# Kernel optimization log

Hardware: AMD Instinct MI355X
Metric: run time of the kernel (lower is better)

The kernel has to match this reference:

```python
import jax, jax.numpy as jnp
import numpy as np

DIM = 768
HEADS = 12
K_PARTS = 64
MLP_HIDDEN = 4 * DIM
EPS = 1e-5


def layer_norm(x, g, b):
    mu = jnp.mean(x, axis=-1, keepdims=True)
    var = jnp.mean(jnp.square(x - mu), axis=-1, keepdims=True)
    return (x - mu) * jax.lax.rsqrt(var + EPS) * g + b


def attention(x, qkv_w, qkv_b, proj_w, proj_b, num_heads):
    B, N, C = x.shape
    hd = C // num_heads
    scale = hd ** -0.5
    qkv = x @ qkv_w.T + qkv_b                      # (B,N,3C)
    qkv = qkv.reshape(B, N, 3, num_heads, hd).transpose(2, 0, 3, 1, 4)  # (3,B,H,N,hd)
    q, k, v = qkv[0], qkv[1], qkv[2]
    attn = jax.nn.softmax(jnp.einsum('bhqd,bhkd->bhqk', q, k) * scale, axis=-1)
    out = jnp.einsum('bhqk,bhkd->bhqd', attn, v)   # (B,H,N,hd)
    out = out.transpose(0, 2, 1, 3).reshape(B, N, C)
    return out @ proj_w.T + proj_b, attn


def mlp(x, fc1_w, fc1_b, fc2_w, fc2_b):
    h = jax.nn.gelu(x @ fc1_w.T + fc1_b, approximate=False)
    return h @ fc2_w.T + fc2_b


def setup_inputs() -> dict:
    key = jax.random.key(0)
    ks = jax.random.split(key, 16)
    s = lambda fan_in: 1.0 / np.sqrt(fan_in)
    inp = {
        'x': jax.random.normal(ks[0], (8, 1024, DIM), dtype=jnp.float32),
        'ln1_g': jnp.ones((DIM,), jnp.float32),
        'ln1_b': jnp.zeros((DIM,), jnp.float32),
        'qkv_w': jax.random.normal(ks[1], (3 * DIM, DIM), jnp.float32) * s(DIM),
        'qkv_b': jnp.zeros((3 * DIM,), jnp.float32),
        'proj_w': jax.random.normal(ks[2], (DIM, DIM), jnp.float32) * s(DIM),
        'proj_b': jnp.zeros((DIM,), jnp.float32),
        'c_qkv_w': jax.random.normal(ks[3], (3 * DIM, DIM), jnp.float32) * s(DIM),
        'c_qkv_b': jnp.zeros((3 * DIM,), jnp.float32),
        'c_proj_w': jax.random.normal(ks[4], (DIM, DIM), jnp.float32) * s(DIM),
        'c_proj_b': jnp.zeros((DIM,), jnp.float32),
        'cp_fc1_w': jax.random.normal(ks[5], (K_PARTS, K_PARTS), jnp.float32) * s(K_PARTS),
        'cp_fc1_b': jnp.zeros((K_PARTS,), jnp.float32),
        'cp_fc2_w': jax.random.normal(ks[6], (DIM, K_PARTS), jnp.float32) * s(K_PARTS),
        'cp_fc2_b': jnp.zeros((DIM,), jnp.float32),
        'P': jax.random.normal(ks[7], (K_PARTS, DIM), jnp.float32),
        'ln2_g': jnp.ones((DIM,), jnp.float32),
        'ln2_b': jnp.zeros((DIM,), jnp.float32),
        'fc1_w': jax.random.normal(ks[8], (MLP_HIDDEN, DIM), jnp.float32) * s(DIM),
        'fc1_b': jnp.zeros((MLP_HIDDEN,), jnp.float32),
        'fc2_w': jax.random.normal(ks[9], (DIM, MLP_HIDDEN), jnp.float32) * s(MLP_HIDDEN),
        'fc2_b': jnp.zeros((DIM,), jnp.float32),
    }
    # normalize P rows like the module init (F.normalize(orthogonal, dim=-1))
    inp['P'] = inp['P'] / jnp.linalg.norm(inp['P'], axis=-1, keepdims=True)
    return inp


def reference(x, ln1_g, ln1_b, qkv_w, qkv_b, proj_w, proj_b,
              c_qkv_w, c_qkv_b, c_proj_w, c_proj_b,
              cp_fc1_w, cp_fc1_b, cp_fc2_w, cp_fc2_b, P,
              ln2_g, ln2_b, fc1_w, fc1_b, fc2_w, fc2_b):
    n1 = layer_norm(x, ln1_g, ln1_b)
    y, _ = attention(n1, qkv_w, qkv_b, proj_w, proj_b, HEADS)
    # SimilarityMaps: L2-normalize tokens and parts, cosine similarity map (B,N,K)
    Un = n1 / jnp.linalg.norm(n1, axis=-1, keepdims=True)
    Pn = P / jnp.linalg.norm(P, axis=-1, keepdims=True)
    dmap = jnp.einsum('bnd,kd->bnk', Un, Pn)
    # c_project: Mlp K -> K -> dim, then parts attention
    zin = mlp(dmap, cp_fc1_w, cp_fc1_b, cp_fc2_w, cp_fc2_b)
    z, _ = attention(zin, c_qkv_w, c_qkv_b, c_proj_w, c_proj_b, HEADS)
    x = x + y + z                                  # gamma_1 is None, drop_path=0
    x = x + mlp(layer_norm(x, ln2_g, ln2_b), fc1_w, fc1_b, fc2_w, fc2_b)
    return x, dmap
```

## Files before the change

kernel.cpp:

```cpp
#include <hip/hip_runtime.h>


typedef unsigned short u16;
typedef unsigned int   u32;
typedef __attribute__((ext_vector_type(8))) short short8;
typedef __attribute__((ext_vector_type(8))) unsigned short ushort8v;
typedef __attribute__((ext_vector_type(4))) float f32x4;

#define F_GELU     1
#define F_ROWSCALE 2
#define F_RES1     4
#define F_RESF     8
#define F_OUTB     16
#define F_OUTF     32
#define F_BIAS     64

__device__ __forceinline__ float bf2f(u32 b) { return __uint_as_float(b << 16); }
__device__ __forceinline__ u16 f2bf(float f) {
    u32 u = __float_as_uint(f);
    u32 r = u + 0x7fffu + ((u >> 16) & 1u);
    return (u16)(r >> 16);
}
__device__ __forceinline__ u16 f2bf_fast(float f) {
    return (u16)((__float_as_uint(f) + 0x8000u) >> 16);
}
__device__ __forceinline__ float gelu_exact(float v) {
    return 0.5f * v * (1.0f + erff(v * 0.70710678118654752440f));
}
__device__ __forceinline__ float gelu_fast(float x) {
    float u = 0.79788456080286535588f * (x + 0.044715f * x * x * x);
    float e = __builtin_amdgcn_exp2f(u * 2.88539008177792681472f);
    float t = 1.0f - 2.0f / (e + 1.0f);
    return 0.5f * x * (1.0f + t);
}

__device__ __forceinline__ void gload16(const u16* g, u16* l) {
    __builtin_amdgcn_global_load_lds(
        (const __attribute__((address_space(1))) u32*)g,
        (__attribute__((address_space(3))) u32*)l, 16, 0, 0);
}

struct ConvArgs {
    const float* src[8];
    u16*         dst[8];
    int          nblk[9];
    int          n[8];
};

__global__ __launch_bounds__(256)
void conv_all_k(ConvArgs a)
{
    const int b = blockIdx.x;
    int i = 0;
    #pragma unroll
    for (int j = 0; j < 7; j++) if (b >= a.nblk[j + 1]) i = j + 1;
    const int base = (b - a.nblk[i]) * 1024 + threadIdx.x * 4;
    if (base >= a.n[i]) return;
    float4 v = *(const float4*)(a.src[i] + base);
    ushort4 o;
    o.x = f2bf(v.x); o.y = f2bf(v.y); o.z = f2bf(v.z); o.w = f2bf(v.w);
    *(ushort4*)(a.dst[i] + base) = o;
}

__device__ __forceinline__ float block_sum(float v, float* red) {
    #pragma unroll
    for (int off = 32; off > 0; off >>= 1) v += __shfl_down(v, off);
    __syncthreads();
    if ((threadIdx.x & 63) == 0) red[threadIdx.x >> 6] = v;
    __syncthreads();
    return red[0] + red[1] + red[2] + red[3];
}

template<bool NORM>
__global__ __launch_bounds__(256)
void ln_k(const float* __restrict__ xin, const float* __restrict__ g,
          const float* __restrict__ bta, u16* __restrict__ out,
          float* __restrict__ invnorm)
{
    __shared__ float red[4];
    const int row = blockIdx.x, t = threadIdx.x;
    float v[3];
    #pragma unroll
    for (int i = 0; i < 3; i++)
        v[i] = xin[(size_t)row * 768 + t + i * 256];
    float tot = block_sum(v[0] + v[1] + v[2], red);
    float mu  = tot * (1.0f / 768.0f);
    float d0 = v[0] - mu, d1 = v[1] - mu, d2 = v[2] - mu;
    float tot2 = block_sum(d0 * d0 + d1 * d1 + d2 * d2, red);
    float rstd = rsqrtf(tot2 * (1.0f / 768.0f) + 1e-5f);
    float ss = 0.0f;
    #pragma unroll
    for (int i = 0; i < 3; i++) {
        int c = t + i * 256;
        float yy = (v[i] - mu) * rstd * g[c] + bta[c];
        out[(size_t)row * 768 + c] = f2bf(yy);
        ss += yy * yy;
    }
    if constexpr (NORM) {
        float tot3 = block_sum(ss, red);
        if (t == 0) invnorm[row] = rsqrtf(tot3);
    }
}

__global__ __launch_bounds__(256)
void pn_k(const float* __restrict__ P, u16* __restrict__ Pn)
{
    __shared__ float red[4];
    const int row = blockIdx.x, t = threadIdx.x;
    float v[3];
    #pragma unroll
    for (int i = 0; i < 3; i++)
        v[i] = P[(size_t)row * 768 + t + i * 256];
    float tot = block_sum(v[0]*v[0] + v[1]*v[1] + v[2]*v[2], red);
    float inv = rsqrtf(tot);
    #pragma unroll
    for (int i = 0; i < 3; i++)
        Pn[(size_t)row * 768 + t + i * 256] = f2bf(v[i] * inv);
}

template<int FLAGS>
__global__ __launch_bounds__(256)
void gemm_mfma(const u16* __restrict__ A, const u16* __restrict__ W,
               const float* __restrict__ bias,
               const u16* __restrict__ res1, const float* __restrict__ resf,
               u16* __restrict__ out, float* __restrict__ outf,
               int M, int N, int K)
{
    __shared__ u16 smem[3][8192];
    const int t = threadIdx.x;
    const int wave = t >> 6, lane = t & 63;
    const int nbx  = gridDim.x;
    const int orig = blockIdx.x + blockIdx.y * nbx;
    const int cpx  = (nbx * gridDim.y) >> 3;
    const int xcd  = orig & 7, loc = orig >> 3;
    const int Rc   = cpx / nbx;
    const int gsz  = 6 * Rc;
    const int grp  = loc / gsz;
    const int rem  = loc - grp * gsz;
    const int ccol = grp * 6 + rem % 6;
    const int crow = xcd * Rc + rem / 6;
    const int m0 = crow * 128, n0 = ccol * 128;
    const int Wm = (wave >> 1) * 64, Wn = (wave & 1) * 64;
    const int rr = lane >> 2, cc = (lane & 3) * 8;
    const int quad = lane >> 4, r16 = lane & 15;
    const int NK = K >> 5;

    f32x4 acc[4][4];
    #pragma unroll
    for (int i = 0; i < 4; i++)
        #pragma unroll
        for (int j = 0; j < 4; j++)
            acc[i][j] = (f32x4){0.f, 0.f, 0.f, 0.f};

    #pragma unroll
    for (int c = 0; c < 2; c++) {
        const int chunk = wave * 2 + c;
        const int row = chunk * 16 + rr;
        gload16(A + (size_t)(m0 + row) * K + cc, &smem[0][chunk * 512]);
        gload16(W + (size_t)(n0 + row) * K + cc, &smem[0][4096 + chunk * 512]);
    }
    if (NK > 1) {
        #pragma unroll
        for (int c = 0; c < 2; c++) {
            const int chunk = wave * 2 + c;
            const int row = chunk * 16 + rr;
            gload16(A + (size_t)(m0 + row) * K + 32 + cc, &smem[1][chunk * 512]);
            gload16(W + (size_t)(n0 + row) * K + 32 + cc, &smem[1][4096 + chunk * 512]);
        }
    }

    for (int kt = 0; kt < NK; kt++) {
        const int cur = kt % 3;
        if (kt + 1 < NK)
            asm volatile("s_waitcnt vmcnt(4)\n\ts_barrier" ::: "memory");
        else
            asm volatile("s_waitcnt vmcnt(0)\n\ts_barrier" ::: "memory");
        if (kt + 2 < NK) {
            const int k0 = (kt + 2) * 32;
            const int nb = (kt + 2) % 3;
            #pragma unroll
            for (int c = 0; c < 2; c++) {
                const int chunk = wave * 2 + c;
                const int row = chunk * 16 + rr;
                gload16(A + (size_t)(m0 + row) * K + k0 + cc,
                        &smem[nb][chunk * 512]);
                gload16(W + (size_t)(n0 + row) * K + k0 + cc,
                        &smem[nb][4096 + chunk * 512]);
            }
        }
        short8 af[4], bfr[4];
        #pragma unroll
        for (int i = 0; i < 4; i++) {
            af[i]  = *(const short8*)&smem[cur][(Wm + i * 16 + r16) * 32 + quad * 8];
            bfr[i] = *(const short8*)&smem[cur][4096 + (Wn + i * 16 + r16) * 32 + quad * 8];
        }
        #pragma unroll
        for (int i = 0; i < 4; i++)
            #pragma unroll
            for (int j = 0; j < 4; j++)
                acc[i][j] = __builtin_amdgcn_mfma_f32_16x16x32_bf16(
                    af[i], bfr[j], acc[i][j], 0, 0, 0);
    }
    __syncthreads();

    float* myl = (float*)&smem[0][0] + wave * 1088;
    float bj[4];
    #pragma unroll
    for (int j = 0; j < 4; j++) {
        if constexpr (FLAGS & F_BIAS) bj[j] = bias[n0 + Wn + j * 16 + r16];
        else bj[j] = 0.0f;
    }
    const int row = lane >> 2, seg = (lane & 3) * 16;

    #pragma unroll
    for (int i = 0; i < 4; i++) {
        #pragma unroll
        for (int j = 0; j < 4; j++)
            #pragma unroll
            for (int r = 0; r < 4; r++) {
                float v = acc[i][j][r] + bj[j];
                if constexpr (FLAGS & F_GELU) v = gelu_fast(v);
                myl[(quad * 4 + r) * 68 + j * 16 + r16] = v;
            }
        float v[16];
        #pragma unroll
        for (int k4 = 0; k4 < 4; k4++) {
            float4 f = *(const float4*)&myl[row * 68 + seg + k4 * 4];
            v[k4 * 4 + 0] = f.x; v[k4 * 4 + 1] = f.y;
            v[k4 * 4 + 2] = f.z; v[k4 * 4 + 3] = f.w;
        }
        const int m = m0 + Wm + i * 16 + row;
        const size_t idx = (size_t)m * N + n0 + Wn + seg;
        if constexpr (FLAGS & F_RES1) {
            ushort8v r0 = *(const ushort8v*)(res1 + idx);
            ushort8v r1 = *(const ushort8v*)(res1 + idx + 8);
            #pragma unroll
            for (int k = 0; k < 8; k++) { v[k] += bf2f(r0[k]); v[k + 8] += bf2f(r1[k]); }
        }
        if constexpr (FLAGS & F_RESF) {
            #pragma unroll
            for (int k4 = 0; k4 < 4; k4++) {
                float4 f = *(const float4*)(resf + idx + k4 * 4);
                v[k4 * 4 + 0] += f.x; v[k4 * 4 + 1] += f.y;
                v[k4 * 4 + 2] += f.z; v[k4 * 4 + 3] += f.w;
            }
        }
        if constexpr (FLAGS & F_OUTB) {
            ushort8v o0, o1;
            #pragma unroll
            for (int k = 0; k < 8; k++) { o0[k] = f2bf(v[k]); o1[k] = f2bf(v[k + 8]); }
            *(ushort8v*)(out + idx) = o0;
            *(ushort8v*)(out + idx + 8) = o1;
        }
        if constexpr (FLAGS & F_OUTF) {
            #pragma unroll
            for (int k4 = 0; k4 < 4; k4++) {
                float4 f = {v[k4 * 4 + 0], v[k4 * 4 + 1], v[k4 * 4 + 2], v[k4 * 4 + 3]};
                *(float4*)(outf + idx + k4 * 4) = f;
            }
        }
    }
}

template<int BM, int BN, int FLAGS>
__global__ __launch_bounds__(256)
void gemm_k(const u16* __restrict__ A, const u16* __restrict__ W,
            const float* __restrict__ bias, const float* __restrict__ rowscale,
            const u16* __restrict__ res1, const float* __restrict__ resf,
            u16* __restrict__ out, float* __restrict__ outf,
            int M, int N, int K)
{
    constexpr int RM = BM / 16, RN = BN / 16;
    __shared__ float Asm[16][BM + 4];
    __shared__ float Wsm[16][BN + 4];
    const int t  = threadIdx.x;
    const int tx = t & 15, ty = t >> 4;
    const int m0 = blockIdx.y * BM, n0 = blockIdx.x * BN;

    float acc[RM][RN];
    #pragma unroll
    for (int i = 0; i < RM; i++)
        #pragma unroll
        for (int j = 0; j < RN; j++) acc[i][j] = 0.0f;

    for (int k0 = 0; k0 < K; k0 += 16) {
        #pragma unroll
        for (int i = 0; i < BM / 64; i++) {
            int f = t + i * 256, r = f >> 2, c4 = (f & 3) << 2;
            uint2 u = *(const uint2*)(A + (size_t)(m0 + r) * K + k0 + c4);
            Asm[c4 + 0][r] = bf2f(u.x & 0xffffu);
            Asm[c4 + 1][r] = bf2f(u.x >> 16);
            Asm[c4 + 2][r] = bf2f(u.y & 0xffffu);
            Asm[c4 + 3][r] = bf2f(u.y >> 16);
        }
        #pragma unroll
        for (int i = 0; i < BN / 64; i++) {
            int f = t + i * 256, r = f >> 2, c4 = (f & 3) << 2;
            uint2 u = *(const uint2*)(W + (size_t)(n0 + r) * K + k0 + c4);
            Wsm[c4 + 0][r] = bf2f(u.x & 0xffffu);
            Wsm[c4 + 1][r] = bf2f(u.x >> 16);
            Wsm[c4 + 2][r] = bf2f(u.y & 0xffffu);
            Wsm[c4 + 3][r] = bf2f(u.y >> 16);
        }
        __syncthreads();
        #pragma unroll
        for (int k = 0; k < 16; k++) {
            float a[RM], w[RN];
            #pragma unroll
            for (int ii = 0; ii < RM; ii += 4) {
                float4 v = *(const float4*)&Asm[k][ty * RM + ii];
                a[ii] = v.x; a[ii + 1] = v.y; a[ii + 2] = v.z; a[ii + 3] = v.w;
            }
            #pragma unroll
            for (int jj = 0; jj < RN; jj += 4) {
                float4 v = *(const float4*)&Wsm[k][tx * RN + jj];
                w[jj] = v.x; w[jj + 1] = v.y; w[jj + 2] = v.z; w[jj + 3] = v.w;
            }
            #pragma unroll
            for (int i = 0; i < RM; i++)
                #pragma unroll
                for (int j = 0; j < RN; j++)
                    acc[i][j] = fmaf(a[i], w[j], acc[i][j]);
        }
        __syncthreads();
    }

    #pragma unroll
    for (int i = 0; i < RM; i++) {
        const int m = m0 + ty * RM + i;
        float rs = 1.0f;
        if constexpr (FLAGS & F_ROWSCALE) rs = rowscale[m];
        #pragma unroll
        for (int jj = 0; jj < RN; jj += 4) {
            const int n = n0 + tx * RN + jj;
            const size_t idx = (size_t)m * N + n;
            float b4[4] = {0.f, 0.f, 0.f, 0.f};
            if constexpr (FLAGS & F_BIAS) {
                float4 bvv = *(const float4*)(bias + n);
                b4[0] = bvv.x; b4[1] = bvv.y; b4[2] = bvv.z; b4[3] = bvv.w;
            }
            float e[4];
            #pragma unroll
            for (int j = 0; j < 4; j++) {
                float v = acc[i][jj + j];
                if constexpr (FLAGS & F_BIAS) v += b4[j];
                if constexpr (FLAGS & F_GELU) v = gelu_exact(v);
                if constexpr (FLAGS & F_ROWSCALE) v *= rs;
                e[j] = v;
            }
            if constexpr (FLAGS & F_OUTB) {
                ushort4 o4;
                o4.x = f2bf(e[0]); o4.y = f2bf(e[1]);
                o4.z = f2bf(e[2]); o4.w = f2bf(e[3]);
                *(ushort4*)(out + idx) = o4;
            }
            if constexpr (FLAGS & F_OUTF) {
                float4 o4 = {e[0], e[1], e[2], e[3]};
                *(float4*)(outf + idx) = o4;
            }
        }
    }
}

__global__ __launch_bounds__(256)
void attn_mfma(const u16* __restrict__ qkv, u16* __restrict__ out)
{
    const int orig = blockIdx.x + blockIdx.y * 8;
    const int wg   = (orig & 7) * 96 + (orig >> 3);
    const int qt = wg & 7;
    const int bh = wg >> 3;
    const int b = bh / 12, h = bh % 12;
    __shared__ u16 Qs[2 * 128 * 32];
    __shared__ u16 Ks[2 * 64 * 32];
    __shared__ u16 Vt[2 * 64 * 32];
    __shared__ u16 Ps[2 * 128 * 32];
    const int t = threadIdx.x;
    const int wave = t >> 6, lane = t & 63;
    const int quad = lane >> 4, r16 = lane & 15;
    const size_t RS = 2304;
    const int tok0 = b * 1024 + qt * 128;
    const u16* qbase = qkv + (size_t)tok0 * RS + h * 64;
    const float SC = 0.125f * 1.44269504088896340736f;

    #pragma unroll
    for (int c = 0; c < 4; c++) {
        int idx = wave * 4 + c;
        int kc = idx >> 3, rg = idx & 7;
        int row = rg * 16 + (lane >> 2);
        gload16(qbase + (size_t)row * RS + kc * 32 + (lane & 3) * 8,
                &Qs[kc * 4096 + rg * 512]);
    }

    f32x4 O[2][4];
    float lpart[2][4];
    #pragma unroll
    for (int i = 0; i < 2; i++)
        #pragma unroll
        for (int j = 0; j < 4; j++) {
            O[i][j] = (f32x4){0.f, 0.f, 0.f, 0.f};
            lpart[i][j & 3] = 0.0f;
        }

    const int kp = t & 63, dg = t >> 6;
    const int vb = (kp >> 5) * 2048 + (kp & 31);
    uint2 vr[4];

    {
        const u16* kbase = qkv + (size_t)(b * 1024) * RS + 768 + h * 64;
        #pragma unroll
        for (int c = 0; c < 2; c++) {
            int idx = wave * 2 + c;
            int kc = idx >> 2, rg = idx & 3;
            int row = rg * 16 + (lane >> 2);
            gload16(kbase + (size_t)row * RS + kc * 32 + (lane & 3) * 8,
                    &Ks[kc * 2048 + rg * 512]);
        }
        const u16* vbase = qkv + (size_t)(b * 1024) * RS + 1536 + h * 64;
        #pragma unroll
        for (int it = 0; it < 4; it++) {
            int d0 = dg * 16 + it * 4;
            vr[it] = *(const uint2*)(vbase + (size_t)kp * RS + d0);
        }
    }

    for (int kt = 0; kt < 16; kt++) {
        __syncthreads();
        #pragma unroll
        for (int it = 0; it < 4; it++) {
            int d0 = dg * 16 + it * 4;
            uint2 u = vr[it];
            Vt[vb + (d0 + 0) * 32] = (u16)(u.x & 0xffffu);
            Vt[vb + (d0 + 1) * 32] = (u16)(u.x >> 16);
            Vt[vb + (d0 + 2) * 32] = (u16)(u.y & 0xffffu);
            Vt[vb + (d0 + 3) * 32] = (u16)(u.y >> 16);
        }

        f32x4 S[2][4];
        #pragma unroll
        for (int i = 0; i < 2; i++)
            #pragma unroll
            for (int j = 0; j < 4; j++)
                S[i][j] = (f32x4){0.f, 0.f, 0.f, 0.f};
        __builtin_amdgcn_s_setprio(1);
        #pragma unroll
        for (int kc = 0; kc < 2; kc++) {
            short8 aq[2], bk[4];
            #pragma unroll
            for (int i = 0; i < 2; i++)
                aq[i] = *(const short8*)&Qs[kc * 4096 + (wave * 32 + i * 16 + r16) * 32 + quad * 8];
            #pragma unroll
            for (int j = 0; j < 4; j++)
                bk[j] = *(const short8*)&Ks[kc * 2048 + (j * 16 + r16) * 32 + quad * 8];
            #pragma unroll
            for (int i = 0; i < 2; i++)
                #pragma unroll
                for (int j = 0; j < 4; j++)
                    S[i][j] = __builtin_amdgcn_mfma_f32_16x16x32_bf16(
                        aq[i], bk[j], S[i][j], 0, 0, 0);
        }
        __builtin_amdgcn_s_setprio(0);

        #pragma unroll
        for (int i = 0; i < 2; i++) {
            #pragma unroll
            for (int j = 0; j < 4; j++) {
                const int col = j * 16 + r16;
                const int pb = (col >> 5) * 4096 + (col & 31);
                #pragma unroll
                for (int r = 0; r < 4; r++) {
                    float p = __builtin_amdgcn_exp2f(S[i][j][r] * SC);
                    lpart[i][r] += p;
                    const int row = wave * 32 + i * 16 + quad * 4 + r;
                    Ps[pb + row * 32] = f2bf_fast(p);
                }
            }
        }

        __syncthreads();

        if (kt < 15) {
            const u16* kbase = qkv + (size_t)(b * 1024 + (kt + 1) * 64) * RS + 768 + h * 64;
            #pragma unroll
            for (int c = 0; c < 2; c++) {
                int idx = wave * 2 + c;
                int kc = idx >> 2, rg = idx & 3;
                int row = rg * 16 + (lane >> 2);
                gload16(kbase + (size_t)row * RS + kc * 32 + (lane & 3) * 8,
                        &Ks[kc * 2048 + rg * 512]);
            }
            const u16* vbase = qkv + (size_t)(b * 1024 + (kt + 1) * 64) * RS + 1536 + h * 64;
            #pragma unroll
            for (int it = 0; it < 4; it++) {
                int d0 = dg * 16 + it * 4;
                vr[it] = *(const uint2*)(vbase + (size_t)kp * RS + d0);
            }
        }

        __builtin_amdgcn_s_setprio(1);
        #pragma unroll
        for (int kc = 0; kc < 2; kc++) {
            short8 ap[2], bv[4];
            #pragma unroll
            for (int i = 0; i < 2; i++)
                ap[i] = *(const short8*)&Ps[kc * 4096 + (wave * 32 + i * 16 + r16) * 32 + quad * 8];
            #pragma unroll
            for (int j = 0; j < 4; j++)
                bv[j] = *(const short8*)&Vt[kc * 2048 + (j * 16 + r16) * 32 + quad * 8];
            #pragma unroll
            for (int i = 0; i < 2; i++)
                #pragma unroll
                for (int j = 0; j < 4; j++)
                    O[i][j] = __builtin_amdgcn_mfma_f32_16x16x32_bf16(
                        ap[i], bv[j], O[i][j], 0, 0, 0);
        }
        __builtin_amdgcn_s_setprio(0);
    }

    const int row = lane >> 2, seg = (lane & 3) * 16;
    #pragma unroll
    for (int i = 0; i < 2; i++) {
        float linv[4];
        #pragma unroll
        for (int r = 0; r < 4; r++) {
            float l = lpart[i][r];
            l += __shfl_xor(l, 1);
            l += __shfl_xor(l, 2);
            l += __shfl_xor(l, 4);
            l += __shfl_xor(l, 8);
            linv[r] = 1.0f / l;
        }
        u16* myl = &Ps[wave * 2048 + i * 1024];
        #pragma unroll
        for (int j = 0; j < 4; j++)
            #pragma unroll
            for (int r = 0; r < 4; r++)
                myl[(quad * 4 + r) * 64 + j * 16 + r16] = f2bf(O[i][j][r] * linv[r]);
        const int token = tok0 + wave * 32 + i * 16 + row;
        const size_t oidx = (size_t)token * 768 + h * 64 + seg;
        *(ushort8v*)(out + oidx)     = *(const ushort8v*)&myl[row * 64 + seg];
        *(ushort8v*)(out + oidx + 8) = *(const ushort8v*)&myl[row * 64 + seg + 8];
    }
}

extern "C" void kernel_launch(void* const* d_in, const int* in_sizes, int n_in,
                              void* d_out, int out_size, void* d_ws, size_t ws_size,
                              hipStream_t stream)
{
    (void)in_sizes; (void)n_in; (void)out_size; (void)ws_size;
    const float* x        = (const float*)d_in[0];
    const float* ln1_g    = (const float*)d_in[1];
    const float* ln1_b    = (const float*)d_in[2];
    const float* qkv_w    = (const float*)d_in[3];
    const float* qkv_b    = (const float*)d_in[4];
    const float* proj_w   = (const float*)d_in[5];
    const float* proj_b   = (const float*)d_in[6];
    const float* c_qkv_w  = (const float*)d_in[7];
    const float* c_qkv_b  = (const float*)d_in[8];
    const float* c_proj_w = (const float*)d_in[9];
    const float* c_proj_b = (const float*)d_in[10];
    const float* cp_fc1_w = (const float*)d_in[11];
    const float* cp_fc1_b = (const float*)d_in[12];
    const float* cp_fc2_w = (const float*)d_in[13];
    const float* cp_fc2_b = (const float*)d_in[14];
    const float* P        = (const float*)d_in[15];
    const float* ln2_g    = (const float*)d_in[16];
    const float* ln2_b    = (const float*)d_in[17];
    const float* fc1_w    = (const float*)d_in[18];
    const float* fc1_b    = (const float*)d_in[19];
    const float* fc2_w    = (const float*)d_in[20];
    const float* fc2_b    = (const float*)d_in[21];

    float* out_x    = (float*)d_out;
    float* out_dmap = out_x + 6291456;

    u16* us    = (u16*)d_ws;
    u16* n1n2  = us;
    u16* bigA  = us + 6291456;
    u16* ao    = bigA + 18874368;
    u16* y     = us + 31457280;
    float* xs  = (float*)(us + 37748736);
    u16* dmapb = us + 50331648;
    u16* cph   = us + 50855936;
    u16* Pn    = us + 51380224;
    float* invn = (float*)(us + 51429376);
    u16* ci    = us + 51445760;

    u16* w_qkv   = ci;
    u16* w_proj  = ci + 1769472;
    u16* w_cqkv  = ci + 2359296;
    u16* w_cproj = ci + 4128768;
    u16* w_cpf1  = ci + 4718592;
    u16* w_cpf2  = ci + 4722688;
    u16* w_fc1   = ci + 4771840;
    u16* w_fc2   = ci + 7131136;

    {
        ConvArgs a;
        const float* wsrc[8] = { qkv_w, proj_w, c_qkv_w, c_proj_w,
                                 cp_fc1_w, cp_fc2_w, fc1_w, fc2_w };
        u16* wdst[8] = { w_qkv, w_proj, w_cqkv, w_cproj,
                         w_cpf1, w_cpf2, w_fc1, w_fc2 };
        const int wn[8] = { 1769472, 589824, 1769472, 589824,
                            4096, 49152, 2359296, 2359296 };
        int cum = 0;
        for (int i = 0; i < 8; i++) {
            a.src[i] = wsrc[i]; a.dst[i] = wdst[i]; a.n[i] = wn[i];
            a.nblk[i] = cum;
            cum += (wn[i] / 4 + 255) / 256;
        }
        a.nblk[8] = cum;
        conv_all_k<<<cum, 256, 0, stream>>>(a);
    }

    pn_k<<<64, 256, 0, stream>>>(P, Pn);
    ln_k<true><<<8192, 256, 0, stream>>>(x, ln1_g, ln1_b, n1n2, invn);
    gemm_mfma<F_BIAS | F_OUTB>
        <<<dim3(18, 64), 256, 0, stream>>>(n1n2, w_qkv, qkv_b, nullptr, nullptr,
                                           bigA, nullptr, 8192, 2304, 768);
    attn_mfma<<<dim3(8, 96), 256, 0, stream>>>(bigA, ao);
    gemm_mfma<F_BIAS | F_OUTB>
        <<<dim3(6, 64), 256, 0, stream>>>(ao, w_proj, proj_b, nullptr, nullptr,
                                          y, nullptr, 8192, 768, 768);
    gemm_k<64, 64, F_ROWSCALE | F_OUTB | F_OUTF>
        <<<dim3(1, 128), 256, 0, stream>>>(n1n2, Pn, nullptr, invn, nullptr,
                                           nullptr, dmapb, out_dmap, 8192, 64, 768);
    gemm_k<64, 64, F_BIAS | F_GELU | F_OUTB>
        <<<dim3(1, 128), 256, 0, stream>>>(dmapb, w_cpf1, cp_fc1_b, nullptr,
                                           nullptr, nullptr, cph, nullptr, 8192, 64, 64);
    gemm_mfma<F_BIAS | F_OUTB>
        <<<dim3(6, 64), 256, 0, stream>>>(cph, w_cpf2, cp_fc2_b, nullptr, nullptr,
                                          n1n2, nullptr, 8192, 768, 64);
    gemm_mfma<F_BIAS | F_OUTB>
        <<<dim3(18, 64), 256, 0, stream>>>(n1n2, w_cqkv, c_qkv_b, nullptr, nullptr,
                                           bigA, nullptr, 8192, 2304, 768);
    attn_mfma<<<dim3(8, 96), 256, 0, stream>>>(bigA, ao);
    gemm_mfma<F_BIAS | F_RES1 | F_RESF | F_OUTF>
        <<<dim3(6, 64), 256, 0, stream>>>(ao, w_cproj, c_proj_b, y, x,
                                          nullptr, xs, 8192, 768, 768);
    ln_k<false><<<8192, 256, 0, stream>>>(xs, ln2_g, ln2_b, n1n2, nullptr);
    gemm_mfma<F_BIAS | F_GELU | F_OUTB>
        <<<dim3(24, 64), 256, 0, stream>>>(n1n2, w_fc1, fc1_b, nullptr, nullptr,
                                           bigA, nullptr, 8192, 3072, 768);
    gemm_mfma<F_BIAS | F_RESF | F_OUTF>
        <<<dim3(6, 64), 256, 0, stream>>>(bigA, w_fc2, fc2_b, nullptr, xs,
                                          nullptr, out_x, 8192, 768, 3072);
}
```

Before: 545.4 us.

## Add 256x256-tile 512-thread MFMA GEMM for QKV and FC1 projections

Adds a new bf16 MFMA GEMM kernel with 256x256 output tiles, 8 waves, double-buffered swizzled LDS, direct global-to-LDS loads and XCD-aware block mapping. It replaces the smaller-tile GEMM for the two QKV projections and FC1. The aim is more data reuse per tile and fewer global loads per FLOP on these large-N GEMMs. The tradeoff is fewer blocks (288/384), which may underfill the GPU's CUs and cause tail effects, plus heavy register use from 128 accumulators per thread.

New measurement: 588.3 us. 7.9% more time.

```diff
diff --git a/kernel.cpp b/kernel.cpp
--- a/kernel.cpp
+++ b/kernel.cpp
@@ -116,6 +116,140 @@
     #pragma unroll
     for (int i = 0; i < 3; i++)
         Pn[(size_t)row * 768 + t + i * 256] = f2bf(v[i] * inv);
+}
+
+template<int FLAGS>
+__global__ __launch_bounds__(512, 2)
+void gemm256(const u16* __restrict__ A, const u16* __restrict__ W,
+             const float* __restrict__ bias, u16* __restrict__ out,
+             int M, int N, int K)
+{
+    __shared__ u16 As[2][16384];
+    __shared__ u16 Bs[2][16384];
+    const int t = threadIdx.x;
+    const int wave = t >> 6, lane = t & 63;
+    const int quad = lane >> 4, r16 = lane & 15;
+    const int wr = wave >> 2, wc = wave & 3;
+
+    const int nbx = gridDim.x, nby = gridDim.y;
+    const int orig = blockIdx.x + blockIdx.y * nbx;
+    const int Rc   = nby >> 3;
+    const int xcd  = orig & 7, loc = orig >> 3;
+    const int m0 = (xcd * Rc + (loc % Rc)) * 256;
+    const int n0 = (loc / Rc) * 256;
+    const int NT = K >> 6;
+
+    f32x4 acc[8][4];
+    #pragma unroll
+    for (int i = 0; i < 8; i++)
+        #pragma unroll
+        for (int j = 0; j < 4; j++)
+            acc[i][j] = (f32x4){0.f, 0.f, 0.f, 0.f};
+
+    const int srow = wave * 8 + (lane >> 3);
+    const int scol = ((lane & 7) ^ ((lane >> 3) & 7)) * 8;
+
+    const u16* Abase = A + (size_t)m0 * K;
+    const u16* Wbase = W + (size_t)n0 * K;
+
+    #pragma unroll
+    for (int i = 0; i < 4; i++)
+        gload16(Abase + (size_t)(i * 64 + srow) * K + scol,
+                &As[0][i * 4096 + wave * 512]);
+    #pragma unroll
+    for (int i = 0; i < 4; i++)
+        gload16(Wbase + (size_t)(i * 64 + srow) * K + scol,
+                &Bs[0][i * 4096 + wave * 512]);
+    if (NT > 1) {
+        #pragma unroll
+        for (int i = 0; i < 4; i++)
+            gload16(Abase + (size_t)(i * 64 + srow) * K + 64 + scol,
+                    &As[1][i * 4096 + wave * 512]);
+        #pragma unroll
+        for (int i = 0; i < 4; i++)
+            gload16(Wbase + (size_t)(i * 64 + srow) * K + 64 + scol,
+                    &Bs[1][i * 4096 + wave * 512]);
+    }
+
+    for (int kt = 0; kt < NT; kt++) {
+        const int c = kt & 1;
+        if (kt + 1 < NT)
+            asm volatile("s_waitcnt vmcnt(8)\n\ts_barrier" ::: "memory");
+        else
+            asm volatile("s_waitcnt vmcnt(0)\n\ts_barrier" ::: "memory");
+
+        #pragma unroll
+        for (int ks = 0; ks < 2; ks++) {
+            short8 bfr[4], af[8];
+            #pragma unroll
+            for (int j = 0; j < 4; j++) {
+                const int br = wc * 64 + j * 16 + r16;
+                bfr[j] = *(const short8*)
+                    &Bs[c][br * 64 + (((ks * 4 + quad) ^ (br & 7)) * 8)];
+            }
+            #pragma unroll
+            for (int i = 0; i < 8; i++) {
+                const int ar = wr * 128 + i * 16 + r16;
+                af[i] = *(const short8*)
+                    &As[c][ar * 64 + (((ks * 4 + quad) ^ (ar & 7)) * 8)];
+            }
+            __builtin_amdgcn_s_setprio(1);
+            #pragma unroll
+            for (int i = 0; i < 8; i++)
+                #pragma unroll
+                for (int j = 0; j < 4; j++)
+                    acc[i][j] = __builtin_amdgcn_mfma_f32_16x16x32_bf16(
+                        af[i], bfr[j], acc[i][j], 0, 0, 0);
+            __builtin_amdgcn_s_setprio(0);
+        }
+        asm volatile("s_barrier" ::: "memory");
+        if (kt + 2 < NT) {
+            const int k0 = (kt + 2) * 64;
+            #pragma unroll
+            for (int i = 0; i < 4; i++)
+                gload16(Abase + (size_t)(i * 64 + srow) * K + k0 + scol,
+                        &As[c][i * 4096 + wave * 512]);
+            #pragma unroll
+            for (int i = 0; i < 4; i++)
+                gload16(Wbase + (size_t)(i * 64 + srow) * K + k0 + scol,
+                        &Bs[c][i * 4096 + wave * 512]);
+        }
+    }
+
+    float* myl = (float*)&As[0][0] + wave * 1088;
+    float bj[4];
+    #pragma unroll
+    for (int j = 0; j < 4; j++) {
+        if constexpr (FLAGS & F_BIAS) bj[j] = bias[n0 + wc * 64 + j * 16 + r16];
+        else bj[j] = 0.0f;
+    }
+    const int row = lane >> 2, seg = (lane & 3) * 16;
+
+    #pragma unroll
+    for (int i = 0; i < 8; i++) {
+        #pragma unroll
+        for (int j = 0; j < 4; j++)
+            #pragma unroll
+            for (int r = 0; r < 4; r++) {
+                float v = acc[i][j][r] + bj[j];
+                if constexpr (FLAGS & F_GELU) v = gelu_fast(v);
+                myl[(quad * 4 + r) * 68 + j * 16 + r16] = v;
+            }
+        float v[16];
+        #pragma unroll
+        for (int k4 = 0; k4 < 4; k4++) {
+            float4 f = *(const float4*)&myl[row * 68 + seg + k4 * 4];
+            v[k4 * 4 + 0] = f.x; v[k4 * 4 + 1] = f.y;
+            v[k4 * 4 + 2] = f.z; v[k4 * 4 + 3] = f.w;
+        }
+        const int m = m0 + wr * 128 + i * 16 + row;
+        const size_t idx = (size_t)m * N + n0 + wc * 64 + seg;
+        ushort8v o0, o1;
+        #pragma unroll
+        for (int k = 0; k < 8; k++) { o0[k] = f2bf(v[k]); o1[k] = f2bf(v[k + 8]); }
+        *(ushort8v*)(out + idx) = o0;
+        *(ushort8v*)(out + idx + 8) = o1;
+    }
 }
 
 template<int FLAGS>
@@ -614,9 +748,9 @@
 
     pn_k<<<64, 256, 0, stream>>>(P, Pn);
     ln_k<true><<<8192, 256, 0, stream>>>(x, ln1_g, ln1_b, n1n2, invn);
-    gemm_mfma<F_BIAS | F_OUTB>
-        <<<dim3(18, 64), 256, 0, stream>>>(n1n2, w_qkv, qkv_b, nullptr, nullptr,
-                                           bigA, nullptr, 8192, 2304, 768);
+    gemm256<F_BIAS | F_OUTB>
+        <<<dim3(9, 32), 512, 0, stream>>>(n1n2, w_qkv, qkv_b, bigA,
+                                          8192, 2304, 768);
     attn_mfma<<<dim3(8, 96), 256, 0, stream>>>(bigA, ao);
     gemm_mfma<F_BIAS | F_OUTB>
         <<<dim3(6, 64), 256, 0, stream>>>(ao, w_proj, proj_b, nullptr, nullptr,
@@ -630,17 +764,17 @@
     gemm_mfma<F_BIAS | F_OUTB>
         <<<dim3(6, 64), 256, 0, stream>>>(cph, w_cpf2, cp_fc2_b, nullptr, nullptr,
                                           n1n2, nullptr, 8192, 768, 64);
-    gemm_mfma<F_BIAS | F_OUTB>
-        <<<dim3(18, 64), 256, 0, stream>>>(n1n2, w_cqkv, c_qkv_b, nullptr, nullptr,
-                                           bigA, nullptr, 8192, 2304, 768);
+    gemm256<F_BIAS | F_OUTB>
+        <<<dim3(9, 32), 512, 0, stream>>>(n1n2, w_cqkv, c_qkv_b, bigA,
+                                          8192, 2304, 768);
     attn_mfma<<<dim3(8, 96), 256, 0, stream>>>(bigA, ao);
     gemm_mfma<F_BIAS | F_RES1 | F_RESF | F_OUTF>
         <<<dim3(6, 64), 256, 0, stream>>>(ao, w_cproj, c_proj_b, y, x,
                                           nullptr, xs, 8192, 768, 768);
     ln_k<false><<<8192, 256, 0, stream>>>(xs, ln2_g, ln2_b, n1n2, nullptr);
-    gemm_mfma<F_BIAS | F_GELU | F_OUTB>
-        <<<dim3(24, 64), 256, 0, stream>>>(n1n2, w_fc1, fc1_b, nullptr, nullptr,
-                                           bigA, nullptr, 8192, 3072, 768);
+    gemm256<F_BIAS | F_GELU | F_OUTB>
+        <<<dim3(12, 32), 512, 0, stream>>>(n1n2, w_fc1, fc1_b, bigA,
+                                           8192, 3072, 768);
     gemm_mfma<F_BIAS | F_RESF | F_OUTF>
         <<<dim3(6, 64), 256, 0, stream>>>(bigA, w_fc2, fc2_b, nullptr, xs,
                                           nullptr, out_x, 8192, 768, 3072);
```
